# Kernel tuning notes

Measured on AMD Instinct MI355X. Metric: run time of the kernel, lower is better.

The kernel has to match this reference:

```python
import jax, jax.numpy as jnp
import numpy as np

N = 10000   # nodes
E = 50000   # edges
C = 64      # in_channels / hidden
OUT = 64    # final out_channels


def _conv(x, src, dst, edge_attr, nn_w, nn_b, lin_w, bias):
    # edge MLP -> per-edge weight matrix [E, C, C]
    W = (edge_attr @ nn_w + nn_b).reshape(-1, C, C)
    x_j = x[src]                                   # gather source features [E, C]
    msg = jnp.einsum('ei,eio->eo', x_j, W)         # batched matvec [E, C]
    out = jax.ops.segment_sum(msg, dst, num_segments=N)  # scatter-add to targets
    out = out + x @ lin_w + bias                   # root weight + bias
    return out


def setup_inputs() -> dict:
    key = jax.random.key(0)
    ks = jax.random.split(key, 13)
    s = 1.0 / np.sqrt(C).astype(np.float32)
    return {
        'feature': jax.random.normal(ks[0], (N, C), dtype=jnp.float32),
        'edge_index': jax.random.randint(ks[1], (2, E), 0, N),
        'edge_attr': jax.random.normal(ks[2], (E, C), dtype=jnp.float32),
        # conv layer 0 (in=64 -> out=64)
        'nn_w0': jax.random.normal(ks[3], (C, C * C), dtype=jnp.float32) * s,
        'nn_b0': jnp.zeros((C * C,), dtype=jnp.float32),
        'lin_w0': jax.random.normal(ks[4], (C, C), dtype=jnp.float32) * s,
        'bias0': jnp.zeros((C,), dtype=jnp.float32),
        # conv layer 1 (64 -> 64)
        'nn_w1': jax.random.normal(ks[5], (C, C * C), dtype=jnp.float32) * s,
        'nn_b1': jnp.zeros((C * C,), dtype=jnp.float32),
        'lin_w1': jax.random.normal(ks[6], (C, C), dtype=jnp.float32) * s,
        'bias1': jnp.zeros((C,), dtype=jnp.float32),
        # final linear 64 -> 64
        'fin_w': jax.random.normal(ks[7], (C, OUT), dtype=jnp.float32) * s,
        'fin_b': jnp.zeros((OUT,), dtype=jnp.float32),
    }


def reference(feature, edge_index, edge_attr,
              nn_w0, nn_b0, lin_w0, bias0,
              nn_w1, nn_b1, lin_w1, bias1,
              fin_w, fin_b):
    src, dst = edge_index[0], edge_index[1]  # PyG flow: source_to_target
    x = jax.nn.relu(_conv(feature, src, dst, edge_attr, nn_w0, nn_b0, lin_w0, bias0))
    x = jax.nn.relu(_conv(x, src, dst, edge_attr, nn_w1, nn_b1, lin_w1, bias1))
    return x @ fin_w + fin_b
```

## Files before the change

### kernel.cpp

```cpp
#include <hip/hip_runtime.h>


#define NNODES 10000
#define NEDGES 50000
#define CH 64
#define NSTAGES 65
#define MW 32

typedef _Float16 f16;
typedef f16 f16x8 __attribute__((ext_vector_type(8)));
typedef float f32x4 __attribute__((ext_vector_type(4)));


__global__ void zero_kernel(int* __restrict__ hist, int* __restrict__ cursor) {
    int idx = blockIdx.x * 256 + threadIdx.x;
    if (idx < NNODES) { hist[idx] = 0; cursor[idx] = 0; }
}

__global__ void hist_kernel(const int* __restrict__ ei, int* __restrict__ hist) {
    int e = blockIdx.x * 256 + threadIdx.x;
    if (e < NEDGES) atomicAdd(&hist[ei[NEDGES + e]], 1);
}

__global__ __launch_bounds__(1024)
void scan_kernel(const int* __restrict__ hist, int* __restrict__ start) {
    __shared__ int buf[1024];
    int t = threadIdx.x;
    int base = t * 10;
    int loc[10];
    int s = 0;
#pragma unroll
    for (int i = 0; i < 10; ++i) {
        int n = base + i;
        int v = (n < NNODES) ? hist[n] : 0;
        loc[i] = s; s += v;
    }
    buf[t] = s;
    __syncthreads();
    for (int off = 1; off < 1024; off <<= 1) {
        int add = (t >= off) ? buf[t - off] : 0;
        __syncthreads();
        buf[t] += add;
        __syncthreads();
    }
    int ebase = buf[t] - s;
#pragma unroll
    for (int i = 0; i < 10; ++i) {
        int n = base + i;
        if (n < NNODES) start[n] = ebase + loc[i];
    }
    if (t == 1023) start[NNODES] = buf[1023];
}

__global__ void perm_kernel(const int* __restrict__ ei,
                            const int* __restrict__ start,
                            int* __restrict__ cursor,
                            int* __restrict__ eperm) {
    int e = blockIdx.x * 256 + threadIdx.x;
    if (e < NEDGES) {
        int d = ei[NEDGES + e];
        int pos = start[d] + atomicAdd(&cursor[d], 1);
        eperm[pos] = e;
    }
}

__global__ void pack_b_kernel(const float* __restrict__ nw0, const float* __restrict__ nb0,
                              const float* __restrict__ nw1, const float* __restrict__ nb1,
                              f16* __restrict__ Bp0, f16* __restrict__ Bp1) {
    int idx = blockIdx.x * 256 + threadIdx.x;
    if (idx >= 2 * NSTAGES * 2048) return;
    int layer = (idx >= NSTAGES * 2048) ? 1 : 0;
    int r = idx - layer * NSTAGES * 2048;
    const float* nn_w = layer ? nw1 : nw0;
    const float* nn_b = layer ? nb1 : nb0;
    f16* Bp = layer ? Bp1 : Bp0;
    int p  = r & 3;
    int f  = r >> 2;
    int ln = f & 63;
    int q2 = (f >> 6) & 7;
    int s  = f >> 9;
    int tn = q2 >> 1, h = q2 & 1;
    int col  = tn * 16 + (ln & 15);
    int koff = h * 32 + (ln >> 4) * 8 + p * 2;
    float v0, v1;
    if (s < 64) {
        v0 = nn_w[(size_t)koff * 4096 + s * 64 + col];
        v1 = nn_w[(size_t)(koff + 1) * 4096 + s * 64 + col];
    } else {
        v0 = nn_b[koff * 64 + col];
        v1 = nn_b[(koff + 1) * 64 + col];
    }
    union { f16 h2[2]; unsigned u; } pk;
    pk.h2[0] = (f16)v0; pk.h2[1] = (f16)v1;
    *(unsigned*)((char*)Bp + (size_t)f * 16 + p * 4) = pk.u;
}

template<bool RELU_IN>
__global__ __launch_bounds__(256)
void root_linear_kernel(const float* __restrict__ x,
                        const float* __restrict__ lw,
                        const float* __restrict__ bias,
                        float* __restrict__ out) {
    int o  = threadIdx.x & 63;
    int gw = (blockIdx.x * 256 + threadIdx.x) >> 6;
    float lwc[64];
#pragma unroll
    for (int k = 0; k < 64; ++k) lwc[k] = lw[k * 64 + o];
    float bo = bias[o];
    for (int n = gw; n < NNODES; n += 1024) {
        const float4* xr = (const float4*)(x + (size_t)n * 64);
        float acc = bo;
#pragma unroll
        for (int kq = 0; kq < 16; ++kq) {
            float4 xv = xr[kq];
            float a = xv.x, b = xv.y, c = xv.z, d = xv.w;
            if (RELU_IN) {
                a = fmaxf(a, 0.f); b = fmaxf(b, 0.f);
                c = fmaxf(c, 0.f); d = fmaxf(d, 0.f);
            }
            acc = fmaf(a, lwc[kq * 4 + 0], acc);
            acc = fmaf(b, lwc[kq * 4 + 1], acc);
            acc = fmaf(c, lwc[kq * 4 + 2], acc);
            acc = fmaf(d, lwc[kq * 4 + 3], acc);
        }
        out[(size_t)n * 64 + o] = acc;
    }
}

template<bool RELU_IN>
__global__ __launch_bounds__(64, 2)
void edge_gemm_kernel(const float* __restrict__ x,
                      const int* __restrict__ ei,
                      const float* __restrict__ ea,
                      const f16* __restrict__ Bp,
                      float* __restrict__ msg) {
    __shared__ f16 xjS[MW][72];

    int ln  = threadIdx.x;
    int l15 = ln & 15, l4 = ln >> 4;
    int e0  = blockIdx.x * MW;

#pragma unroll
    for (int r = 0; r < 8; ++r) {
        int idx = r * 64 + ln;
        int el = idx >> 4, ip = idx & 15;
        int e  = e0 + el;
        float4 v = {0.f, 0.f, 0.f, 0.f};
        if (e < NEDGES)
            v = *(const float4*)(x + (size_t)ei[e] * CH + ip * 4);
        if (RELU_IN) {
            v.x = fmaxf(v.x, 0.f); v.y = fmaxf(v.y, 0.f);
            v.z = fmaxf(v.z, 0.f); v.w = fmaxf(v.w, 0.f);
        }
        union { f16 h4[4]; uint2 u; } pk;
        pk.h4[0] = (f16)v.x; pk.h4[1] = (f16)v.y;
        pk.h4[2] = (f16)v.z; pk.h4[3] = (f16)v.w;
        *(uint2*)&xjS[el][ip * 4] = pk.u;
    }

    f16x8 eav[2][2];
#pragma unroll
    for (int ms = 0; ms < 2; ++ms) {
        int e = e0 + ms * 16 + l15;
#pragma unroll
        for (int h = 0; h < 2; ++h) {
            float4 a = {0.f,0.f,0.f,0.f}, b = {0.f,0.f,0.f,0.f};
            if (e < NEDGES) {
                const float4* p = (const float4*)(ea + (size_t)e * CH + h * 32 + l4 * 8);
                a = p[0]; b = p[1];
            }
            f16x8 f;
            f[0]=(f16)a.x; f[1]=(f16)a.y; f[2]=(f16)a.z; f[3]=(f16)a.w;
            f[4]=(f16)b.x; f[5]=(f16)b.y; f[6]=(f16)b.z; f[7]=(f16)b.w;
            eav[ms][h] = f;
        }
    }

    f32x4 acc[2][4];
#pragma unroll
    for (int ms = 0; ms < 2; ++ms)
#pragma unroll
        for (int tn = 0; tn < 4; ++tn)
            acc[ms][tn] = (f32x4){0.f, 0.f, 0.f, 0.f};

    const char* gB = (const char*)Bp + ln * 16;

#define LOADB(b, sidx) do {                                                     \
        const char* _p = gB + (size_t)(sidx) * 8192;                            \
        _Pragma("unroll")                                                       \
        for (int q2 = 0; q2 < 8; ++q2)                                          \
            b[q2] = *(const f16x8*)(_p + q2 * 1024);                            \
    } while (0)

#define COMP(sidx, b) do {                                                      \
        f16 _x0 = xjS[l15][(sidx)];                                             \
        f16 _x1 = xjS[16 + l15][(sidx)];                                        \
        f16x8 _xs0 = {_x0,_x0,_x0,_x0,_x0,_x0,_x0,_x0};                         \
        f16x8 _xs1 = {_x1,_x1,_x1,_x1,_x1,_x1,_x1,_x1};                         \
        _Pragma("unroll")                                                       \
        for (int h = 0; h < 2; ++h) {                                           \
            f16x8 _a0 = eav[0][h] * _xs0;                                       \
            f16x8 _a1 = eav[1][h] * _xs1;                                       \
            _Pragma("unroll")                                                   \
            for (int tn = 0; tn < 4; ++tn) {                                    \
                acc[0][tn] = __builtin_amdgcn_mfma_f32_16x16x32_f16(_a0, b[tn*2+h], acc[0][tn], 0, 0, 0); \
                acc[1][tn] = __builtin_amdgcn_mfma_f32_16x16x32_f16(_a1, b[tn*2+h], acc[1][tn], 0, 0, 0); \
            }                                                                   \
        }                                                                       \
    } while (0)

    f16x8 b0[8], b1[8], b2[8];
    LOADB(b0, 0); LOADB(b1, 1); LOADB(b2, 2);

#pragma unroll 1
    for (int s = 0; s < 63; s += 3) {
        COMP(s,     b0); LOADB(b0, min(s + 3, 64));
        COMP(s + 1, b1); LOADB(b1, min(s + 4, 64));
        COMP(s + 2, b2); LOADB(b2, min(s + 5, 64));
    }
    COMP(63, b0);
#pragma unroll
    for (int ms = 0; ms < 2; ++ms)
#pragma unroll
        for (int h = 0; h < 2; ++h) {
            f16x8 af = *(const f16x8*)&xjS[ms * 16 + l15][h * 32 + l4 * 8];
#pragma unroll
            for (int tn = 0; tn < 4; ++tn)
                acc[ms][tn] = __builtin_amdgcn_mfma_f32_16x16x32_f16(af, b1[tn * 2 + h], acc[ms][tn], 0, 0, 0);
        }

#pragma unroll
    for (int ms = 0; ms < 2; ++ms)
#pragma unroll
        for (int q = 0; q < 4; ++q) {
            int e = e0 + ms * 16 + l4 * 4 + q;
            if (e < NEDGES) {
                float* row = msg + (size_t)e * CH;
#pragma unroll
                for (int tn = 0; tn < 4; ++tn)
                    row[tn * 16 + l15] = acc[ms][tn][q];
            }
        }
#undef LOADB
#undef COMP
}

__global__ __launch_bounds__(256)
void reduce_kernel(float* __restrict__ buf,
                   const float* __restrict__ msg,
                   const int* __restrict__ start,
                   const int* __restrict__ eperm) {
    int gw = (blockIdx.x * 256 + threadIdx.x) >> 6;
    int o  = threadIdx.x & 63;
    if (gw >= NNODES) return;
    float acc = buf[(size_t)gw * CH + o];
    int b = start[gw], e = start[gw + 1];
    for (int p = b; p < e; ++p) {
        int ed = eperm[p];
        acc += msg[(size_t)ed * CH + o];
    }
    buf[(size_t)gw * CH + o] = acc;
}

extern "C" void kernel_launch(void* const* d_in, const int* in_sizes, int n_in,
                              void* d_out, int out_size, void* d_ws, size_t ws_size,
                              hipStream_t stream) {
    const float* feature = (const float*)d_in[0];
    const int*   ei      = (const int*)d_in[1];
    const float* ea      = (const float*)d_in[2];
    const float* nn_w0   = (const float*)d_in[3];
    const float* nn_b0   = (const float*)d_in[4];
    const float* lin_w0  = (const float*)d_in[5];
    const float* bias0   = (const float*)d_in[6];
    const float* nn_w1   = (const float*)d_in[7];
    const float* nn_b1   = (const float*)d_in[8];
    const float* lin_w1  = (const float*)d_in[9];
    const float* bias1   = (const float*)d_in[10];
    const float* fin_w   = (const float*)d_in[11];
    const float* fin_b   = (const float*)d_in[12];
    float* out = (float*)d_out;

    char* ws = (char*)d_ws;
    float* buf0   = (float*)(ws + 0);
    float* buf1   = (float*)(ws + 2560000);
    f16*   Bp0    = (f16*)  (ws + 5120000);
    f16*   Bp1    = (f16*)  (ws + 5652480);
    int*   hist   = (int*)  (ws + 6184960);
    int*   cursor = (int*)  (ws + 6224960);
    int*   startp = (int*)  (ws + 6264960);
    int*   eperm  = (int*)  (ws + 6304976);
    float* msg    = (float*)(ws + 6504976);

    zero_kernel<<<(NNODES + 255) / 256, 256, 0, stream>>>(hist, cursor);
    hist_kernel<<<(NEDGES + 255) / 256, 256, 0, stream>>>(ei, hist);
    scan_kernel<<<1, 1024, 0, stream>>>(hist, startp);
    perm_kernel<<<(NEDGES + 255) / 256, 256, 0, stream>>>(ei, startp, cursor, eperm);

    int pack_blocks = (2 * NSTAGES * 2048 + 255) / 256;
    pack_b_kernel<<<pack_blocks, 256, 0, stream>>>(nn_w0, nn_b0, nn_w1, nn_b1, Bp0, Bp1);

    dim3 eg((NEDGES + MW - 1) / MW);

    root_linear_kernel<false><<<256, 256, 0, stream>>>(feature, lin_w0, bias0, buf0);
    edge_gemm_kernel<false><<<eg, 64, 0, stream>>>(feature, ei, ea, Bp0, msg);
    reduce_kernel<<<(NNODES * CH + 255) / 256, 256, 0, stream>>>(buf0, msg, startp, eperm);
    root_linear_kernel<true><<<256, 256, 0, stream>>>(buf0, lin_w1, bias1, buf1);
    edge_gemm_kernel<true><<<eg, 64, 0, stream>>>(buf0, ei, ea, Bp1, msg);
    reduce_kernel<<<(NNODES * CH + 255) / 256, 256, 0, stream>>>(buf1, msg, startp, eperm);
    root_linear_kernel<true><<<256, 256, 0, stream>>>(buf1, fin_w, fin_b, out);
}
```

Baseline: 158.7 us.

## Fuse root linear with segment reduce, widen edge tiles to 64 edges

Merges the root-weight linear and the CSR segment reduction into one kernel, removing a separate reduce pass and one read/write round trip of the node buffers. The edge GEMM kernel now handles 64 edges per block with four M-subtiles, so each loaded weight stage is reused across twice as many edges. Explicit s_waitcnt plus sched_barrier calls pin the order of the triple-buffered weight loads. The larger tile raises register pressure, which may cut occupancy, and halves the number of blocks.

New measurement: 206.1 us. 29.9% more time.

```diff
diff --git a/kernel.cpp b/kernel.cpp
--- a/kernel.cpp
+++ b/kernel.cpp
@@ -5,7 +5,7 @@
 #define NEDGES 50000
 #define CH 64
 #define NSTAGES 65
-#define MW 32
+#define MW 64
 
 typedef _Float16 f16;
 typedef f16 f16x8 __attribute__((ext_vector_type(8)));
@@ -96,11 +96,143 @@
 }
 
 template<bool RELU_IN>
+__global__ __launch_bounds__(64, 2)
+void edge_gemm_kernel(const float* __restrict__ x,
+                      const int* __restrict__ ei,
+                      const float* __restrict__ ea,
+                      const f16* __restrict__ Bp,
+                      float* __restrict__ msg) {
+    __shared__ f16 xjS[MW][72];
+
+    int ln  = threadIdx.x;
+    int l15 = ln & 15, l4 = ln >> 4;
+    int e0  = blockIdx.x * MW;
+
+#pragma unroll
+    for (int r = 0; r < 16; ++r) {
+        int idx = r * 64 + ln;
+        int el = idx >> 4, ip = idx & 15;
+        int e  = e0 + el;
+        float4 v = {0.f, 0.f, 0.f, 0.f};
+        if (e < NEDGES)
+            v = *(const float4*)(x + (size_t)ei[e] * CH + ip * 4);
+        if (RELU_IN) {
+            v.x = fmaxf(v.x, 0.f); v.y = fmaxf(v.y, 0.f);
+            v.z = fmaxf(v.z, 0.f); v.w = fmaxf(v.w, 0.f);
+        }
+        union { f16 h4[4]; uint2 u; } pk;
+        pk.h4[0] = (f16)v.x; pk.h4[1] = (f16)v.y;
+        pk.h4[2] = (f16)v.z; pk.h4[3] = (f16)v.w;
+        *(uint2*)&xjS[el][ip * 4] = pk.u;
+    }
+
+    f16x8 eav[4][2];
+#pragma unroll
+    for (int ms = 0; ms < 4; ++ms) {
+        int e = e0 + ms * 16 + l15;
+#pragma unroll
+        for (int h = 0; h < 2; ++h) {
+            float4 a = {0.f,0.f,0.f,0.f}, b = {0.f,0.f,0.f,0.f};
+            if (e < NEDGES) {
+                const float4* p = (const float4*)(ea + (size_t)e * CH + h * 32 + l4 * 8);
+                a = p[0]; b = p[1];
+            }
+            f16x8 f;
+            f[0]=(f16)a.x; f[1]=(f16)a.y; f[2]=(f16)a.z; f[3]=(f16)a.w;
+            f[4]=(f16)b.x; f[5]=(f16)b.y; f[6]=(f16)b.z; f[7]=(f16)b.w;
+            eav[ms][h] = f;
+        }
+    }
+
+    f32x4 acc[4][4];
+#pragma unroll
+    for (int ms = 0; ms < 4; ++ms)
+#pragma unroll
+        for (int tn = 0; tn < 4; ++tn)
+            acc[ms][tn] = (f32x4){0.f, 0.f, 0.f, 0.f};
+
+    const char* gB = (const char*)Bp + ln * 16;
+
+#define LOADB(b, sidx) do {                                                     \
+        const char* _p = gB + (size_t)(sidx) * 8192;                            \
+        _Pragma("unroll")                                                       \
+        for (int q2 = 0; q2 < 8; ++q2)                                          \
+            b[q2] = *(const f16x8*)(_p + q2 * 1024);                            \
+    } while (0)
+
+#define COMP(sidx, b) do {                                                      \
+        f16x8 xsp[4];                                                           \
+        _Pragma("unroll")                                                       \
+        for (int ms = 0; ms < 4; ++ms) {                                        \
+            f16 xv = xjS[ms * 16 + l15][(sidx)];                                \
+            xsp[ms] = (f16x8){xv, xv, xv, xv, xv, xv, xv, xv};                  \
+        }                                                                       \
+        _Pragma("unroll")                                                       \
+        for (int ms = 0; ms < 4; ++ms) {                                        \
+            f16x8 a0 = eav[ms][0] * xsp[ms];                                    \
+            f16x8 a1 = eav[ms][1] * xsp[ms];                                    \
+            _Pragma("unroll")                                                   \
+            for (int tn = 0; tn < 4; ++tn) {                                    \
+                acc[ms][tn] = __builtin_amdgcn_mfma_f32_16x16x32_f16(a0, b[tn*2+0], acc[ms][tn], 0, 0, 0); \
+                acc[ms][tn] = __builtin_amdgcn_mfma_f32_16x16x32_f16(a1, b[tn*2+1], acc[ms][tn], 0, 0, 0); \
+            }                                                                   \
+        }                                                                       \
+    } while (0)
+
+#define WAIT16 do { asm volatile("s_waitcnt vmcnt(16)" ::: "memory");           \
+                    __builtin_amdgcn_sched_barrier(0); } while (0)
+
+    f16x8 b0[8], b1[8], b2[8];
+    LOADB(b0, 0); LOADB(b1, 1); LOADB(b2, 2);
+    asm volatile("s_waitcnt vmcnt(0)" ::: "memory");
+    __builtin_amdgcn_sched_barrier(0);
+
+#pragma unroll 1
+    for (int s = 0; s < 63; s += 3) {
+        WAIT16; COMP(s,     b0); LOADB(b0, s + 3);
+        WAIT16; COMP(s + 1, b1); LOADB(b1, s + 4);
+        WAIT16; COMP(s + 2, b2); LOADB(b2, min(s + 5, 64));
+    }
+    WAIT16;
+    COMP(63, b0);
+    asm volatile("s_waitcnt vmcnt(8)" ::: "memory");
+    __builtin_amdgcn_sched_barrier(0);
+#pragma unroll
+    for (int ms = 0; ms < 4; ++ms)
+#pragma unroll
+        for (int h = 0; h < 2; ++h) {
+            f16x8 af = *(const f16x8*)&xjS[ms * 16 + l15][h * 32 + l4 * 8];
+#pragma unroll
+            for (int tn = 0; tn < 4; ++tn)
+                acc[ms][tn] = __builtin_amdgcn_mfma_f32_16x16x32_f16(af, b1[tn * 2 + h], acc[ms][tn], 0, 0, 0);
+        }
+
+#pragma unroll
+    for (int ms = 0; ms < 4; ++ms)
+#pragma unroll
+        for (int q = 0; q < 4; ++q) {
+            int e = e0 + ms * 16 + l4 * 4 + q;
+            if (e < NEDGES) {
+                float* row = msg + (size_t)e * CH;
+#pragma unroll
+                for (int tn = 0; tn < 4; ++tn)
+                    row[tn * 16 + l15] = acc[ms][tn][q];
+            }
+        }
+#undef LOADB
+#undef COMP
+#undef WAIT16
+}
+
+template<bool RELU_IN>
 __global__ __launch_bounds__(256)
-void root_linear_kernel(const float* __restrict__ x,
-                        const float* __restrict__ lw,
-                        const float* __restrict__ bias,
-                        float* __restrict__ out) {
+void rootreduce_kernel(const float* __restrict__ x,
+                       const float* __restrict__ lw,
+                       const float* __restrict__ bias,
+                       const float* __restrict__ msg,
+                       const int* __restrict__ start,
+                       const int* __restrict__ eperm,
+                       float* __restrict__ outb) {
     int o  = threadIdx.x & 63;
     int gw = (blockIdx.x * 256 + threadIdx.x) >> 6;
     float lwc[64];
@@ -123,143 +255,37 @@
             acc = fmaf(c, lwc[kq * 4 + 2], acc);
             acc = fmaf(d, lwc[kq * 4 + 3], acc);
         }
+        int pb = start[n], pe = start[n + 1];
+        for (int p = pb; p < pe; ++p)
+            acc += msg[(size_t)eperm[p] * 64 + o];
+        outb[(size_t)n * 64 + o] = acc;
+    }
+}
+
+__global__ __launch_bounds__(256)
+void final_kernel(const float* __restrict__ x,
+                  const float* __restrict__ fw,
+                  const float* __restrict__ fb,
+                  float* __restrict__ out) {
+    int o  = threadIdx.x & 63;
+    int gw = (blockIdx.x * 256 + threadIdx.x) >> 6;
+    float fwc[64];
+#pragma unroll
+    for (int k = 0; k < 64; ++k) fwc[k] = fw[k * 64 + o];
+    float bo = fb[o];
+    for (int n = gw; n < NNODES; n += 1024) {
+        const float4* xr = (const float4*)(x + (size_t)n * 64);
+        float acc = bo;
+#pragma unroll
+        for (int kq = 0; kq < 16; ++kq) {
+            float4 xv = xr[kq];
+            acc = fmaf(fmaxf(xv.x, 0.f), fwc[kq * 4 + 0], acc);
+            acc = fmaf(fmaxf(xv.y, 0.f), fwc[kq * 4 + 1], acc);
+            acc = fmaf(fmaxf(xv.z, 0.f), fwc[kq * 4 + 2], acc);
+            acc = fmaf(fmaxf(xv.w, 0.f), fwc[kq * 4 + 3], acc);
+        }
         out[(size_t)n * 64 + o] = acc;
     }
-}
-
-template<bool RELU_IN>
-__global__ __launch_bounds__(64, 2)
-void edge_gemm_kernel(const float* __restrict__ x,
-                      const int* __restrict__ ei,
-                      const float* __restrict__ ea,
-                      const f16* __restrict__ Bp,
-                      float* __restrict__ msg) {
-    __shared__ f16 xjS[MW][72];
-
-    int ln  = threadIdx.x;
-    int l15 = ln & 15, l4 = ln >> 4;
-    int e0  = blockIdx.x * MW;
-
-#pragma unroll
-    for (int r = 0; r < 8; ++r) {
-        int idx = r * 64 + ln;
-        int el = idx >> 4, ip = idx & 15;
-        int e  = e0 + el;
-        float4 v = {0.f, 0.f, 0.f, 0.f};
-        if (e < NEDGES)
-            v = *(const float4*)(x + (size_t)ei[e] * CH + ip * 4);
-        if (RELU_IN) {
-            v.x = fmaxf(v.x, 0.f); v.y = fmaxf(v.y, 0.f);
-            v.z = fmaxf(v.z, 0.f); v.w = fmaxf(v.w, 0.f);
-        }
-        union { f16 h4[4]; uint2 u; } pk;
-        pk.h4[0] = (f16)v.x; pk.h4[1] = (f16)v.y;
-        pk.h4[2] = (f16)v.z; pk.h4[3] = (f16)v.w;
-        *(uint2*)&xjS[el][ip * 4] = pk.u;
-    }
-
-    f16x8 eav[2][2];
-#pragma unroll
-    for (int ms = 0; ms < 2; ++ms) {
-        int e = e0 + ms * 16 + l15;
-#pragma unroll
-        for (int h = 0; h < 2; ++h) {
-            float4 a = {0.f,0.f,0.f,0.f}, b = {0.f,0.f,0.f,0.f};
-            if (e < NEDGES) {
-                const float4* p = (const float4*)(ea + (size_t)e * CH + h * 32 + l4 * 8);
-                a = p[0]; b = p[1];
-            }
-            f16x8 f;
-            f[0]=(f16)a.x; f[1]=(f16)a.y; f[2]=(f16)a.z; f[3]=(f16)a.w;
-            f[4]=(f16)b.x; f[5]=(f16)b.y; f[6]=(f16)b.z; f[7]=(f16)b.w;
-            eav[ms][h] = f;
-        }
-    }
-
-    f32x4 acc[2][4];
-#pragma unroll
-    for (int ms = 0; ms < 2; ++ms)
-#pragma unroll
-        for (int tn = 0; tn < 4; ++tn)
-            acc[ms][tn] = (f32x4){0.f, 0.f, 0.f, 0.f};
-
-    const char* gB = (const char*)Bp + ln * 16;
-
-#define LOADB(b, sidx) do {                                                     \
-        const char* _p = gB + (size_t)(sidx) * 8192;                            \
-        _Pragma("unroll")                                                       \
-        for (int q2 = 0; q2 < 8; ++q2)                                          \
-            b[q2] = *(const f16x8*)(_p + q2 * 1024);                            \
-    } while (0)
-
-#define COMP(sidx, b) do {                                                      \
-        f16 _x0 = xjS[l15][(sidx)];                                             \
-        f16 _x1 = xjS[16 + l15][(sidx)];                                        \
-        f16x8 _xs0 = {_x0,_x0,_x0,_x0,_x0,_x0,_x0,_x0};                         \
-        f16x8 _xs1 = {_x1,_x1,_x1,_x1,_x1,_x1,_x1,_x1};                         \
-        _Pragma("unroll")                                                       \
-        for (int h = 0; h < 2; ++h) {                                           \
-            f16x8 _a0 = eav[0][h] * _xs0;                                       \
-            f16x8 _a1 = eav[1][h] * _xs1;                                       \
-            _Pragma("unroll")                                                   \
-            for (int tn = 0; tn < 4; ++tn) {                                    \
-                acc[0][tn] = __builtin_amdgcn_mfma_f32_16x16x32_f16(_a0, b[tn*2+h], acc[0][tn], 0, 0, 0); \
-                acc[1][tn] = __builtin_amdgcn_mfma_f32_16x16x32_f16(_a1, b[tn*2+h], acc[1][tn], 0, 0, 0); \
-            }                                                                   \
-        }                                                                       \
-    } while (0)
-
-    f16x8 b0[8], b1[8], b2[8];
-    LOADB(b0, 0); LOADB(b1, 1); LOADB(b2, 2);
-
-#pragma unroll 1
-    for (int s = 0; s < 63; s += 3) {
-        COMP(s,     b0); LOADB(b0, min(s + 3, 64));
-        COMP(s + 1, b1); LOADB(b1, min(s + 4, 64));
-        COMP(s + 2, b2); LOADB(b2, min(s + 5, 64));
-    }
-    COMP(63, b0);
-#pragma unroll
-    for (int ms = 0; ms < 2; ++ms)
-#pragma unroll
-        for (int h = 0; h < 2; ++h) {
-            f16x8 af = *(const f16x8*)&xjS[ms * 16 + l15][h * 32 + l4 * 8];
-#pragma unroll
-            for (int tn = 0; tn < 4; ++tn)
-                acc[ms][tn] = __builtin_amdgcn_mfma_f32_16x16x32_f16(af, b1[tn * 2 + h], acc[ms][tn], 0, 0, 0);
-        }
-
-#pragma unroll
-    for (int ms = 0; ms < 2; ++ms)
-#pragma unroll
-        for (int q = 0; q < 4; ++q) {
-            int e = e0 + ms * 16 + l4 * 4 + q;
-            if (e < NEDGES) {
-                float* row = msg + (size_t)e * CH;
-#pragma unroll
-                for (int tn = 0; tn < 4; ++tn)
-                    row[tn * 16 + l15] = acc[ms][tn][q];
-            }
-        }
-#undef LOADB
-#undef COMP
-}
-
-__global__ __launch_bounds__(256)
-void reduce_kernel(float* __restrict__ buf,
-                   const float* __restrict__ msg,
-                   const int* __restrict__ start,
-                   const int* __restrict__ eperm) {
-    int gw = (blockIdx.x * 256 + threadIdx.x) >> 6;
-    int o  = threadIdx.x & 63;
-    if (gw >= NNODES) return;
-    float acc = buf[(size_t)gw * CH + o];
-    int b = start[gw], e = start[gw + 1];
-    for (int p = b; p < e; ++p) {
-        int ed = eperm[p];
-        acc += msg[(size_t)ed * CH + o];
-    }
-    buf[(size_t)gw * CH + o] = acc;
 }
 
 extern "C" void kernel_launch(void* const* d_in, const int* in_sizes, int n_in,
@@ -296,16 +322,16 @@
     scan_kernel<<<1, 1024, 0, stream>>>(hist, startp);
     perm_kernel<<<(NEDGES + 255) / 256, 256, 0, stream>>>(ei, startp, cursor, eperm);
 
-    int pack_blocks = (2 * NSTAGES * 2048 + 255) / 256;
-    pack_b_kernel<<<pack_blocks, 256, 0, stream>>>(nn_w0, nn_b0, nn_w1, nn_b1, Bp0, Bp1);
+    pack_b_kernel<<<(2 * NSTAGES * 2048 + 255) / 256, 256, 0, stream>>>(
+        nn_w0, nn_b0, nn_w1, nn_b1, Bp0, Bp1);
 
     dim3 eg((NEDGES + MW - 1) / MW);
 
-    root_linear_kernel<false><<<256, 256, 0, stream>>>(feature, lin_w0, bias0, buf0);
     edge_gemm_kernel<false><<<eg, 64, 0, stream>>>(feature, ei, ea, Bp0, msg);
-    reduce_kernel<<<(NNODES * CH + 255) / 256, 256, 0, stream>>>(buf0, msg, startp, eperm);
-    root_linear_kernel<true><<<256, 256, 0, stream>>>(buf0, lin_w1, bias1, buf1);
+    rootreduce_kernel<false><<<256, 256, 0, stream>>>(feature, lin_w0, bias0,
+                                                      msg, startp, eperm, buf0);
     edge_gemm_kernel<true><<<eg, 64, 0, stream>>>(buf0, ei, ea, Bp1, msg);
-    reduce_kernel<<<(NNODES * CH + 255) / 256, 256, 0, stream>>>(buf1, msg, startp, eperm);
-    root_linear_kernel<true><<<256, 256, 0, stream>>>(buf1, fin_w, fin_b, out);
-}
+    rootreduce_kernel<true><<<256, 256, 0, stream>>>(buf0, lin_w1, bias1,
+                                                     msg, startp, eperm, buf1);
+    final_kernel<<<256, 256, 0, stream>>>(buf1, fin_w, fin_b, out);
+}
```
